# Kernel tuning notes

Measured on AMD Instinct MI355X. Metric: run time of the kernel, lower is better.

The kernel has to match this reference:

```python
import jax, jax.numpy as jnp
import numpy as np

B, S, D, H = 2, 2048, 1024, 16
DK = D // H

def setup_inputs() -> dict:
    key = jax.random.key(0)
    ks = jax.random.split(key, 8)
    scale = 1.0 / np.sqrt(D)
    return {
        "q": jax.random.normal(ks[0], (B, S, D), jnp.float32),
        "k": jax.random.normal(ks[1], (B, S, D), jnp.float32),
        "v": jax.random.normal(ks[2], (B, S, D), jnp.float32),
        "reaches": jax.random.uniform(ks[3], (B, S), jnp.float32),
        "Wq": jax.random.normal(ks[4], (D, D), jnp.float32) * scale,
        "Wk": jax.random.normal(ks[5], (D, D), jnp.float32) * scale,
        "Wv": jax.random.normal(ks[6], (D, D), jnp.float32) * scale,
        "Wo": jax.random.normal(ks[7], (D, D), jnp.float32) * scale,
    }

def _split_heads(x):
    # [B,S,D] -> [B,H,S,DK]
    return x.reshape(B, S, H, DK).transpose(0, 2, 1, 3)

def reference(q, k, v, reaches, Wq, Wk, Wv, Wo):
    # torch Linear: y = x @ W.T
    qh = _split_heads(q @ Wq.T)
    kh = _split_heads(k @ Wk.T)
    vh = _split_heads(v @ Wv.T)
    scores = jnp.einsum("bhqd,bhkd->bhqk", qh, kh) / jnp.sqrt(jnp.float32(DK))
    scores = jax.nn.softmax(scores, axis=-1)
    # post-softmax reach weighting along key axis
    scores = scores * reaches[:, None, None, :]
    # diagonal suppression: scores - scores*0.999999*eye
    scores = scores * (1.0 - 0.999999 * jnp.eye(S, dtype=scores.dtype))
    # inverted combine
    out = vh - jnp.einsum("bhqk,bhkd->bhqd", scores, vh)
    # per-position contribution rescale
    rs = reaches.sum(axis=-1, keepdims=True)
    contrib = (rs - reaches) / (rs + 1e-9) * (1.0 - reaches) * 100.0  # [B,S]
    out = out * contrib[:, None, :, None]
    concat = out.transpose(0, 2, 1, 3).reshape(B, S, D)
    return concat @ Wo.T
```

## Files before the change

### kernel.cpp

```cpp
#include <hip/hip_runtime.h>
#include <hip/hip_bf16.h>

typedef __attribute__((ext_vector_type(8))) short short8;
typedef __attribute__((ext_vector_type(4))) float f32x4;
typedef __attribute__((ext_vector_type(16))) float f32x16;
typedef unsigned short us;

#define B_ 2
#define S_ 2048
#define D_ 1024
#define H_ 16
#define DK_ 64
#define QSCALE 0.1803368867f

__device__ __forceinline__ us f2bf(float f) {
  union { float f; unsigned u; } x; x.f = f;
  unsigned r = x.u + 0x7FFFu + ((x.u >> 16) & 1u);
  return (us)(r >> 16);
}
__device__ __forceinline__ float bf2f(us h) {
  union { unsigned u; float f; } x; x.u = ((unsigned)h) << 16;
  return x.f;
}
__device__ __forceinline__ us f2bf_hw(float f) {
  __hip_bfloat16 h = __float2bfloat16(f);
  return *reinterpret_cast<us*>(&h);
}
__device__ __forceinline__ unsigned cvtpk(float lo, float hi) {
  unsigned r;
  asm("v_cvt_pk_bf16_f32 %0, %1, %2" : "=v"(r) : "v"(lo), "v"(hi));
  return r;
}

__device__ __forceinline__ void gload16(const void* g, void* l) {
  __builtin_amdgcn_global_load_lds((const __attribute__((address_space(1))) void*)g,
                                   (__attribute__((address_space(3))) void*)l, 16, 0, 0);
}

__global__ __launch_bounds__(256) void cvt_all(const float* __restrict__ q,
                                               const float* __restrict__ k,
                                               const float* __restrict__ v,
                                               const float* __restrict__ Wq,
                                               const float* __restrict__ Wk,
                                               const float* __restrict__ Wv,
                                               const float* __restrict__ Wo,
                                               const float* __restrict__ reaches,
                                               us* __restrict__ oq, us* __restrict__ ok,
                                               us* __restrict__ ov, us* __restrict__ oWq,
                                               us* __restrict__ oWk, us* __restrict__ oWv,
                                               us* __restrict__ oWo, float* __restrict__ rs) {
  int bid = blockIdx.x;
  if (bid >= 16384) {
    __shared__ float tmp[4];
    int t = threadIdx.x;
    for (int b = 0; b < B_; ++b) {
      float s = 0.f;
      for (int i = t; i < S_; i += 256) s += reaches[b * S_ + i];
      for (int o = 32; o > 0; o >>= 1) s += __shfl_down(s, o, 64);
      if ((t & 63) == 0) tmp[t >> 6] = s;
      __syncthreads();
      if (t == 0) rs[b] = tmp[0] + tmp[1] + tmp[2] + tmp[3];
      __syncthreads();
    }
    return;
  }
  const float* in; us* out; int off;
  if (bid < 12288) {
    int t = bid >> 12;
    in = (t == 0) ? q : (t == 1) ? k : v;
    out = (t == 0) ? oq : (t == 1) ? ok : ov;
    off = (bid & 4095) * 1024;
  } else {
    int t = (bid - 12288) >> 10;
    in = (t == 0) ? Wq : (t == 1) ? Wk : (t == 2) ? Wv : Wo;
    out = (t == 0) ? oWq : (t == 1) ? oWk : (t == 2) ? oWv : oWo;
    off = ((bid - 12288) & 1023) * 1024;
  }
  int i = off + threadIdx.x * 4;
  float4 val = *reinterpret_cast<const float4*>(in + i);
  ushort4 o;
  o.x = f2bf(val.x); o.y = f2bf(val.y); o.z = f2bf(val.z); o.w = f2bf(val.w);
  *reinterpret_cast<ushort4*>(out + i) = o;
}

__device__ __forceinline__ void gemm_core_hs(const us* __restrict__ A, const us* __restrict__ Bt,
                                             us* __restrict__ outH, float oscale) {
  __shared__ __align__(16) us lA[3][128 * 32];
  __shared__ __align__(16) us lB[3][128 * 32];
  const int tid = threadIdx.x;
  const int swz = (blockIdx.x & 7) * 32 + (blockIdx.x >> 3);
  const int bm = swz >> 3, bn = swz & 7;
  const int w = tid >> 6, lane = tid & 63;
  const int wr = (w >> 1) * 64, wc = (w & 1) * 64;
  const int lr = lane & 15, lg = lane >> 4;

  f32x4 acc[4][4];
#pragma unroll
  for (int i = 0; i < 4; ++i)
#pragma unroll
    for (int j = 0; j < 4; ++j) acc[i][j] = (f32x4){0.f, 0.f, 0.f, 0.f};

  const int crow = lane >> 2, ce8 = (lane & 3) * 8;
  const us* A0 = A + (size_t)(bm * 128 + w * 32 + crow) * 1024 + ce8;
  const us* A1 = A0 + (size_t)16 * 1024;
  const us* B0 = Bt + (size_t)(bn * 128 + w * 32 + crow) * 1024 + ce8;
  const us* B1 = B0 + (size_t)16 * 1024;
  const int dA0 = (w * 32) * 32, dA1 = (w * 32 + 16) * 32;

  gload16(A0, &lA[0][dA0]);
  gload16(A1, &lA[0][dA1]);
  gload16(B0, &lB[0][dA0]);
  gload16(B1, &lB[0][dA1]);

  int cur = 0, nxt = 1;
  for (int kt = 0; kt < 32; ++kt) {
    if (kt < 31) {
      int ko = (kt + 1) * 32;
      gload16(A0 + ko, &lA[nxt][dA0]);
      gload16(A1 + ko, &lA[nxt][dA1]);
      gload16(B0 + ko, &lB[nxt][dA0]);
      gload16(B1 + ko, &lB[nxt][dA1]);
      asm volatile("s_waitcnt vmcnt(4)" ::: "memory");
    } else {
      asm volatile("s_waitcnt vmcnt(0)" ::: "memory");
    }
    __builtin_amdgcn_s_barrier();
    __builtin_amdgcn_sched_barrier(0);

    short8 af[4], bfr[4];
#pragma unroll
    for (int i = 0; i < 4; ++i)
      af[i] = *reinterpret_cast<const short8*>(&lA[cur][(wr + i * 16 + lr) * 32 + lg * 8]);
#pragma unroll
    for (int j = 0; j < 4; ++j)
      bfr[j] = *reinterpret_cast<const short8*>(&lB[cur][(wc + j * 16 + lr) * 32 + lg * 8]);
    __builtin_amdgcn_s_setprio(1);
#pragma unroll
    for (int i = 0; i < 4; ++i)
#pragma unroll
      for (int j = 0; j < 4; ++j)
        acc[i][j] = __builtin_amdgcn_mfma_f32_16x16x32_bf16(af[i], bfr[j], acc[i][j], 0, 0, 0);
    __builtin_amdgcn_s_setprio(0);

    cur = nxt;
    nxt = (nxt == 2) ? 0 : nxt + 1;
  }
#pragma unroll
  for (int i = 0; i < 4; ++i)
#pragma unroll
    for (int j = 0; j < 4; ++j)
#pragma unroll
      for (int ii = 0; ii < 4; ++ii) {
        int r = bm * 128 + wr + i * 16 + lg * 4 + ii;
        int c = bn * 128 + wc + j * 16 + lr;
        float v = acc[i][j][ii] * oscale;
        int b = r >> 11, s = r & (S_ - 1), h = c >> 6, dk = c & 63;
        outH[(((size_t)(b * H_ + h) * S_ + s) * DK_) + dk] = f2bf(v);
      }
}

__global__ __launch_bounds__(256) void proj_gemm(const us* __restrict__ q_bf,
                                                 const us* __restrict__ k_bf,
                                                 const us* __restrict__ v_bf,
                                                 const us* __restrict__ Wq_bf,
                                                 const us* __restrict__ Wk_bf,
                                                 const us* __restrict__ Wv_bf,
                                                 us* __restrict__ Qh, us* __restrict__ Kh,
                                                 us* __restrict__ Vh) {
  if (blockIdx.y == 0) gemm_core_hs(q_bf, Wq_bf, Qh, QSCALE);
  else if (blockIdx.y == 1) gemm_core_hs(k_bf, Wk_bf, Kh, 1.0f);
  else gemm_core_hs(v_bf, Wv_bf, Vh, 1.0f);
}

__global__ __launch_bounds__(256) void wo_gemm(const us* __restrict__ A,
                                               const us* __restrict__ Bt,
                                               float* __restrict__ outF) {
  __shared__ __align__(16) us lA[3][128 * 32];
  __shared__ __align__(16) us lB[3][64 * 32];
  const int tid = threadIdx.x;
  const int swz = (blockIdx.x & 7) * 64 + (blockIdx.x >> 3);
  const int bm = swz >> 4, bn = swz & 15;
  const int w = tid >> 6, lane = tid & 63;
  const int lr = lane & 15, lg = lane >> 4;

  f32x4 acc[2][4];
#pragma unroll
  for (int i = 0; i < 2; ++i)
#pragma unroll
    for (int j = 0; j < 4; ++j) acc[i][j] = (f32x4){0.f, 0.f, 0.f, 0.f};

  const int crow = lane >> 2, ce8 = (lane & 3) * 8;
  const us* A0 = A + (size_t)(bm * 128 + w * 32 + crow) * 1024 + ce8;
  const us* A1 = A0 + (size_t)16 * 1024;
  const us* B0 = Bt + (size_t)(bn * 64 + w * 16 + crow) * 1024 + ce8;
  const int dA0 = (w * 32) * 32, dA1 = (w * 32 + 16) * 32, dB0 = (w * 16) * 32;

  gload16(A0, &lA[0][dA0]);
  gload16(A1, &lA[0][dA1]);
  gload16(B0, &lB[0][dB0]);

  int cur = 0, nxt = 1;
  for (int kt = 0; kt < 32; ++kt) {
    if (kt < 31) {
      int ko = (kt + 1) * 32;
      gload16(A0 + ko, &lA[nxt][dA0]);
      gload16(A1 + ko, &lA[nxt][dA1]);
      gload16(B0 + ko, &lB[nxt][dB0]);
      asm volatile("s_waitcnt vmcnt(3)" ::: "memory");
    } else {
      asm volatile("s_waitcnt vmcnt(0)" ::: "memory");
    }
    __builtin_amdgcn_s_barrier();
    __builtin_amdgcn_sched_barrier(0);

    short8 af[2], bfr[4];
#pragma unroll
    for (int i = 0; i < 2; ++i)
      af[i] = *reinterpret_cast<const short8*>(&lA[cur][(w * 32 + i * 16 + lr) * 32 + lg * 8]);
#pragma unroll
    for (int j = 0; j < 4; ++j)
      bfr[j] = *reinterpret_cast<const short8*>(&lB[cur][(j * 16 + lr) * 32 + lg * 8]);
    __builtin_amdgcn_s_setprio(1);
#pragma unroll
    for (int i = 0; i < 2; ++i)
#pragma unroll
      for (int j = 0; j < 4; ++j)
        acc[i][j] = __builtin_amdgcn_mfma_f32_16x16x32_bf16(af[i], bfr[j], acc[i][j], 0, 0, 0);
    __builtin_amdgcn_s_setprio(0);

    cur = nxt;
    nxt = (nxt == 2) ? 0 : nxt + 1;
  }
#pragma unroll
  for (int i = 0; i < 2; ++i)
#pragma unroll
    for (int j = 0; j < 4; ++j)
#pragma unroll
      for (int ii = 0; ii < 4; ++ii) {
        int r = bm * 128 + w * 32 + i * 16 + lg * 4 + ii;
        int c = bn * 64 + j * 16 + lr;
        outF[(size_t)r * 1024 + c] = acc[i][j][ii];
      }
}

__global__ __launch_bounds__(256) void transp_kernel(const us* __restrict__ Vh,
                                                     const float* __restrict__ reaches,
                                                     us* __restrict__ VhTw) {
  __shared__ us t[64 * 68];
  const int bh = blockIdx.x >> 5, st = blockIdx.x & 31;
  const int b = bh >> 4;
  const size_t base = (size_t)bh * S_ * DK_;
  const int r = threadIdx.x >> 3, e8 = (threadIdx.x & 7) * 8;
#pragma unroll
  for (int h2 = 0; h2 < 2; ++h2) {
    int row = r + h2 * 32;
    *reinterpret_cast<short8*>(&t[row * 68 + e8]) =
        *reinterpret_cast<const short8*>(&Vh[base + (size_t)(st * 64 + row) * DK_ + e8]);
  }
  __syncthreads();
#pragma unroll
  for (int h2 = 0; h2 < 2; ++h2) {
    int dk = (threadIdx.x >> 3) + h2 * 32;
    int sc = (threadIdx.x & 7) * 8;
    short8 v;
#pragma unroll
    for (int j = 0; j < 8; ++j) {
      float rw = reaches[b * S_ + st * 64 + sc + j];
      v[j] = (short)f2bf_hw(bf2f(t[(sc + j) * 68 + dk]) * rw);
    }
    *reinterpret_cast<short8*>(&VhTw[base + (size_t)dk * S_ + st * 64 + sc]) = v;
  }
}

__global__ __launch_bounds__(256, 2) void attn_kernel(const us* __restrict__ Qh,
                                                      const us* __restrict__ Kh,
                                                      const us* __restrict__ Vh,
                                                      const us* __restrict__ VhTw,
                                                      const float* __restrict__ reaches,
                                                      const float* __restrict__ rsum,
                                                      us* __restrict__ concat) {
  __shared__ __align__(16) us lK2[2][64 * 64];
  __shared__ __align__(16) us vT2[2][64 * 64];
  __shared__ float diagP[128];
  __shared__ float lsum[128];

  const int tid = threadIdx.x;
  const int bid = ((blockIdx.x & 7) << 6) | (blockIdx.x >> 3);
  const int qt = bid & 15;
  const int bh = bid >> 4;
  const int b = bh >> 4, h = bh & 15;
  const size_t base = (size_t)bh * S_ * DK_;

  const int w = tid >> 6, lane = tid & 63;
  const int l31 = lane & 31, hh = lane >> 5, l7 = lane & 7;
  const int h4 = hh * 4;
  const int r2 = tid >> 3, e8 = (tid & 7) * 8;
  const int diagkt = qt * 2 + (w >> 1);

  short8 aq[4];
  {
    const us* qp = &Qh[base + (size_t)(qt * 128 + w * 32 + l31) * DK_ + hh * 8];
#pragma unroll
    for (int dk = 0; dk < 4; ++dk)
      aq[dk] = *reinterpret_cast<const short8*>(qp + dk * 16);
  }

  int rdK[2][4];
#pragma unroll
  for (int c = 0; c < 2; ++c)
#pragma unroll
    for (int dk = 0; dk < 4; ++dk)
      rdK[c][dk] = (c * 32 + l31) * 64 + (((dk * 2 + hh) ^ l7) << 3);
  const int wslot = ((tid & 7) ^ (r2 & 7)) << 3;
  const int wK0 = r2 * 64 + wslot, wK1 = (r2 + 32) * 64 + wslot;

  short8 pk0, pk1, pv0, pv1;
  pk0 = *reinterpret_cast<const short8*>(&Kh[base + (size_t)r2 * DK_ + e8]);
  pk1 = *reinterpret_cast<const short8*>(&Kh[base + (size_t)(r2 + 32) * DK_ + e8]);
  pv0 = *reinterpret_cast<const short8*>(&VhTw[base + (size_t)r2 * S_ + e8]);
  pv1 = *reinterpret_cast<const short8*>(&VhTw[base + (size_t)(r2 + 32) * S_ + e8]);
  *reinterpret_cast<short8*>(&lK2[0][wK0]) = pk0;
  *reinterpret_cast<short8*>(&lK2[0][wK1]) = pk1;
  *reinterpret_cast<short8*>(&vT2[0][wK0]) = pv0;
  *reinterpret_cast<short8*>(&vT2[0][wK1]) = pv1;
  __syncthreads();

  f32x16 oacc[2];
  float lacc = 0.f;
#pragma unroll
  for (int c = 0; c < 2; ++c)
#pragma unroll
    for (int r = 0; r < 16; ++r) oacc[c][r] = 0.f;

  for (int kt = 0; kt < 32; ++kt) {
    const int cur = kt & 1;
    if (kt < 31) {
      int nt = kt + 1;
      pk0 = *reinterpret_cast<const short8*>(&Kh[base + (size_t)(nt * 64 + r2) * DK_ + e8]);
      pk1 = *reinterpret_cast<const short8*>(&Kh[base + (size_t)(nt * 64 + r2 + 32) * DK_ + e8]);
      pv0 = *reinterpret_cast<const short8*>(&VhTw[base + (size_t)r2 * S_ + nt * 64 + e8]);
      pv1 = *reinterpret_cast<const short8*>(&VhTw[base + (size_t)(r2 + 32) * S_ + nt * 64 + e8]);
    }

    f32x16 st0, st1;
#pragma unroll
    for (int r = 0; r < 16; ++r) { st0[r] = 0.f; st1[r] = 0.f; }
    __builtin_amdgcn_s_setprio(1);
#pragma unroll
    for (int dk = 0; dk < 4; ++dk) {
      short8 k0 = *reinterpret_cast<const short8*>(&lK2[cur][rdK[0][dk]]);
      st0 = __builtin_amdgcn_mfma_f32_32x32x16_bf16(k0, aq[dk], st0, 0, 0, 0);
      short8 k1 = *reinterpret_cast<const short8*>(&lK2[cur][rdK[1][dk]]);
      st1 = __builtin_amdgcn_mfma_f32_32x32x16_bf16(k1, aq[dk], st1, 0, 0, 0);
    }
    __builtin_amdgcn_s_setprio(0);

    float e0[16], e1[16];
#pragma unroll
    for (int r = 0; r < 16; ++r) {
      e0[r] = __builtin_amdgcn_exp2f(st0[r]);
      e1[r] = __builtin_amdgcn_exp2f(st1[r]);
      lacc += e0[r] + e1[r];
    }
    if (kt == diagkt) {
#pragma unroll
      for (int r = 0; r < 16; ++r) {
        int kk = (r & 3) + 8 * (r >> 2) + 4 * hh;
        float ev = (w & 1) ? e1[r] : e0[r];
        if (kk == l31) diagP[w * 32 + l31] = ev;
      }
    }

    short8 pa[4];
#pragma unroll
    for (int ks = 0; ks < 4; ++ks) {
      const int ro = (ks & 1) * 8;
      unsigned d0, s0, d1, s1;
      if (ks < 2) {
        d0 = cvtpk(e0[ro + 0], e0[ro + 1]);
        s0 = cvtpk(e0[ro + 4], e0[ro + 5]);
        d1 = cvtpk(e0[ro + 2], e0[ro + 3]);
        s1 = cvtpk(e0[ro + 6], e0[ro + 7]);
      } else {
        d0 = cvtpk(e1[ro + 0], e1[ro + 1]);
        s0 = cvtpk(e1[ro + 4], e1[ro + 5]);
        d1 = cvtpk(e1[ro + 2], e1[ro + 3]);
        s1 = cvtpk(e1[ro + 6], e1[ro + 7]);
      }
      asm("v_permlane32_swap_b32 %0, %1" : "+v"(d0), "+v"(s0));
      asm("v_permlane32_swap_b32 %0, %1" : "+v"(d1), "+v"(s1));
      union { unsigned u[4]; short8 v; } pk;
      pk.u[0] = d0; pk.u[1] = d1; pk.u[2] = s0; pk.u[3] = s1;
      pa[ks] = pk.v;
    }

    __builtin_amdgcn_s_setprio(1);
#pragma unroll
    for (int dc = 0; dc < 2; ++dc)
#pragma unroll
      for (int ks = 0; ks < 4; ++ks) {
        short8 bv = *reinterpret_cast<const short8*>(&vT2[cur][rdK[dc][ks]]);
        oacc[dc] = __builtin_amdgcn_mfma_f32_32x32x16_bf16(pa[ks], bv, oacc[dc], 0, 0, 0);
      }
    __builtin_amdgcn_s_setprio(0);

    if (kt < 31) {
      const int nx = cur ^ 1;
      *reinterpret_cast<short8*>(&lK2[nx][wK0]) = pk0;
      *reinterpret_cast<short8*>(&lK2[nx][wK1]) = pk1;
      *reinterpret_cast<short8*>(&vT2[nx][wK0]) = pv0;
      *reinterpret_cast<short8*>(&vT2[nx][wK1]) = pv1;
    }
    __syncthreads();
  }

  lacc += __shfl_xor(lacc, 32, 64);
  if (hh == 0) lsum[w * 32 + l31] = lacc;
  __syncthreads();

  const float rb = rsum[b];
#pragma unroll
  for (int r = 0; r < 16; ++r) {
    const int q = w * 32 + (r & 3) + 8 * (r >> 2) + h4;
    const int qg = qt * 128 + q;
    const float rq = reaches[b * S_ + qg];
    const float contrib = (rb - rq) / (rb + 1e-9f) * (1.f - rq) * 100.f;
    const float corr = 0.999999f * diagP[q] * rq;
    const float linv = 1.0f / lsum[q];
#pragma unroll
    for (int dc = 0; dc < 2; ++dc) {
      int d = dc * 32 + l31;
      float vhv = bf2f(Vh[base + (size_t)qg * DK_ + d]);
      float pv = (oacc[dc][r] - corr * vhv) * linv;
      float o = (vhv - pv) * contrib;
      concat[((size_t)(b * S_ + qg)) * D_ + h * 64 + d] = f2bf(o);
    }
  }
}

extern "C" void kernel_launch(void* const* d_in, const int* in_sizes, int n_in,
                              void* d_out, int out_size, void* d_ws, size_t ws_size,
                              hipStream_t stream) {
  const float* q = (const float*)d_in[0];
  const float* k = (const float*)d_in[1];
  const float* v = (const float*)d_in[2];
  const float* reaches = (const float*)d_in[3];
  const float* Wq = (const float*)d_in[4];
  const float* Wk = (const float*)d_in[5];
  const float* Wv = (const float*)d_in[6];
  const float* Wo = (const float*)d_in[7];

  const size_t NQKV = (size_t)B_ * S_ * D_;
  const size_t NW = (size_t)D_ * D_;

  us* q_bf = (us*)d_ws;
  us* k_bf = q_bf + NQKV;
  us* v_bf = k_bf + NQKV;
  us* Wq_bf = v_bf + NQKV;
  us* Wk_bf = Wq_bf + NW;
  us* Wv_bf = Wk_bf + NW;
  us* Wo_bf = Wv_bf + NW;
  us* Qh = Wo_bf + NW;
  us* Kh = Qh + NQKV;
  us* Vh = Kh + NQKV;
  us* concat = Vh + NQKV;
  float* rs = (float*)(concat + NQKV);
  us* VhTw = q_bf;

  cvt_all<<<16385, 256, 0, stream>>>(q, k, v, Wq, Wk, Wv, Wo, reaches,
                                     q_bf, k_bf, v_bf, Wq_bf, Wk_bf, Wv_bf, Wo_bf, rs);

  proj_gemm<<<dim3(256, 3), 256, 0, stream>>>(q_bf, k_bf, v_bf, Wq_bf, Wk_bf, Wv_bf, Qh, Kh, Vh);
  transp_kernel<<<B_ * H_ * (S_ / 64), 256, 0, stream>>>(Vh, reaches, VhTw);

  attn_kernel<<<B_ * H_ * (S_ / 128), 256, 0, stream>>>(Qh, Kh, Vh, VhTw, reaches, rs, concat);

  wo_gemm<<<512, 256, 0, stream>>>(concat, Wo_bf, (float*)d_out);
}
```

Measured before the change: 127.2 us.

## Fuse reach-weighted V transpose into V projection GEMM epilogue

```diff
diff --git a/kernel.cpp b/kernel.cpp
--- a/kernel.cpp
+++ b/kernel.cpp
@@ -84,9 +84,10 @@
 }
 
 __device__ __forceinline__ void gemm_core_hs(const us* __restrict__ A, const us* __restrict__ Bt,
-                                             us* __restrict__ outH, float oscale) {
-  __shared__ __align__(16) us lA[3][128 * 32];
-  __shared__ __align__(16) us lB[3][128 * 32];
+                                             us* __restrict__ outH, float oscale,
+                                             const float* __restrict__ reaches,
+                                             us* __restrict__ VhTw, int dov) {
+  __shared__ __align__(16) us smem[3][8192];
   const int tid = threadIdx.x;
   const int swz = (blockIdx.x & 7) * 32 + (blockIdx.x >> 3);
   const int bm = swz >> 3, bn = swz & 7;
@@ -107,19 +108,19 @@
   const us* B1 = B0 + (size_t)16 * 1024;
   const int dA0 = (w * 32) * 32, dA1 = (w * 32 + 16) * 32;
 
-  gload16(A0, &lA[0][dA0]);
-  gload16(A1, &lA[0][dA1]);
-  gload16(B0, &lB[0][dA0]);
-  gload16(B1, &lB[0][dA1]);
+  gload16(A0, &smem[0][dA0]);
+  gload16(A1, &smem[0][dA1]);
+  gload16(B0, &smem[0][4096 + dA0]);
+  gload16(B1, &smem[0][4096 + dA1]);
 
   int cur = 0, nxt = 1;
   for (int kt = 0; kt < 32; ++kt) {
     if (kt < 31) {
       int ko = (kt + 1) * 32;
-      gload16(A0 + ko, &lA[nxt][dA0]);
-      gload16(A1 + ko, &lA[nxt][dA1]);
-      gload16(B0 + ko, &lB[nxt][dA0]);
-      gload16(B1 + ko, &lB[nxt][dA1]);
+      gload16(A0 + ko, &smem[nxt][dA0]);
+      gload16(A1 + ko, &smem[nxt][dA1]);
+      gload16(B0 + ko, &smem[nxt][4096 + dA0]);
+      gload16(B1 + ko, &smem[nxt][4096 + dA1]);
       asm volatile("s_waitcnt vmcnt(4)" ::: "memory");
     } else {
       asm volatile("s_waitcnt vmcnt(0)" ::: "memory");
@@ -130,10 +131,10 @@
     short8 af[4], bfr[4];
 #pragma unroll
     for (int i = 0; i < 4; ++i)
-      af[i] = *reinterpret_cast<const short8*>(&lA[cur][(wr + i * 16 + lr) * 32 + lg * 8]);
+      af[i] = *reinterpret_cast<const short8*>(&smem[cur][(wr + i * 16 + lr) * 32 + lg * 8]);
 #pragma unroll
     for (int j = 0; j < 4; ++j)
-      bfr[j] = *reinterpret_cast<const short8*>(&lB[cur][(wc + j * 16 + lr) * 32 + lg * 8]);
+      bfr[j] = *reinterpret_cast<const short8*>(&smem[cur][4096 + (wc + j * 16 + lr) * 32 + lg * 8]);
     __builtin_amdgcn_s_setprio(1);
 #pragma unroll
     for (int i = 0; i < 4; ++i)
@@ -145,18 +146,53 @@
     cur = nxt;
     nxt = (nxt == 2) ? 0 : nxt + 1;
   }
+
+  us* tbuf = &smem[0][0];
+  if (dov) __syncthreads();
+
 #pragma unroll
   for (int i = 0; i < 4; ++i)
 #pragma unroll
     for (int j = 0; j < 4; ++j)
 #pragma unroll
       for (int ii = 0; ii < 4; ++ii) {
-        int r = bm * 128 + wr + i * 16 + lg * 4 + ii;
-        int c = bn * 128 + wc + j * 16 + lr;
+        int rl = wr + i * 16 + lg * 4 + ii;
+        int cl = wc + j * 16 + lr;
+        int r = bm * 128 + rl;
+        int c = bn * 128 + cl;
         float v = acc[i][j][ii] * oscale;
         int b = r >> 11, s = r & (S_ - 1), h = c >> 6, dk = c & 63;
-        outH[(((size_t)(b * H_ + h) * S_ + s) * DK_) + dk] = f2bf(v);
+        us bv = f2bf(v);
+        outH[(((size_t)(b * H_ + h) * S_ + s) * DK_) + dk] = bv;
+        if (dov) tbuf[cl * 136 + rl] = bv;
       }
+
+  if (dov) {
+    __syncthreads();
+    const int dl = tid >> 1, s0q = (tid & 1) * 64;
+    const int bq = bm >> 4;
+    const int bh = bq * 16 + bn * 2 + (dl >> 6);
+    const int dk = dl & 63;
+    const int sbase = (bm & 15) * 128 + s0q;
+    const size_t ob = (size_t)bh * DK_ * S_ + (size_t)dk * S_ + sbase;
+    const float* rp = reaches + bq * S_ + sbase;
+#pragma unroll
+    for (int k8 = 0; k8 < 8; ++k8) {
+      short8 vv = *reinterpret_cast<const short8*>(&tbuf[dl * 136 + s0q + k8 * 8]);
+      float4 ra = *reinterpret_cast<const float4*>(rp + k8 * 8);
+      float4 rb = *reinterpret_cast<const float4*>(rp + k8 * 8 + 4);
+      short8 ov;
+      ov[0] = (short)f2bf_hw(bf2f((us)vv[0]) * ra.x);
+      ov[1] = (short)f2bf_hw(bf2f((us)vv[1]) * ra.y);
+      ov[2] = (short)f2bf_hw(bf2f((us)vv[2]) * ra.z);
+      ov[3] = (short)f2bf_hw(bf2f((us)vv[3]) * ra.w);
+      ov[4] = (short)f2bf_hw(bf2f((us)vv[4]) * rb.x);
+      ov[5] = (short)f2bf_hw(bf2f((us)vv[5]) * rb.y);
+      ov[6] = (short)f2bf_hw(bf2f((us)vv[6]) * rb.z);
+      ov[7] = (short)f2bf_hw(bf2f((us)vv[7]) * rb.w);
+      *reinterpret_cast<short8*>(&VhTw[ob + k8 * 8]) = ov;
+    }
+  }
 }
 
 __global__ __launch_bounds__(256) void proj_gemm(const us* __restrict__ q_bf,
@@ -166,10 +202,12 @@
                                                  const us* __restrict__ Wk_bf,
                                                  const us* __restrict__ Wv_bf,
                                                  us* __restrict__ Qh, us* __restrict__ Kh,
-                                                 us* __restrict__ Vh) {
-  if (blockIdx.y == 0) gemm_core_hs(q_bf, Wq_bf, Qh, QSCALE);
-  else if (blockIdx.y == 1) gemm_core_hs(k_bf, Wk_bf, Kh, 1.0f);
-  else gemm_core_hs(v_bf, Wv_bf, Vh, 1.0f);
+                                                 us* __restrict__ Vh,
+                                                 const float* __restrict__ reaches,
+                                                 us* __restrict__ VhTw, int dov) {
+  if (blockIdx.y == 0) gemm_core_hs(q_bf, Wq_bf, Qh, QSCALE, nullptr, nullptr, 0);
+  else if (blockIdx.y == 1) gemm_core_hs(k_bf, Wk_bf, Kh, 1.0f, nullptr, nullptr, 0);
+  else gemm_core_hs(v_bf, Wv_bf, Vh, 1.0f, reaches, VhTw, dov);
 }
 
 __global__ __launch_bounds__(256) void wo_gemm(const us* __restrict__ A,
@@ -465,13 +503,19 @@
   us* Vh = Kh + NQKV;
   us* concat = Vh + NQKV;
   float* rs = (float*)(concat + NQKV);
-  us* VhTw = q_bf;
+
+  us* vt_new = (us*)(rs + 4);
+  size_t need = (size_t)((char*)(vt_new + NQKV) - (char*)d_ws);
+  int fused = (ws_size >= need) ? 1 : 0;
+  us* VhTw = fused ? vt_new : q_bf;
 
   cvt_all<<<16385, 256, 0, stream>>>(q, k, v, Wq, Wk, Wv, Wo, reaches,
                                      q_bf, k_bf, v_bf, Wq_bf, Wk_bf, Wv_bf, Wo_bf, rs);
 
-  proj_gemm<<<dim3(256, 3), 256, 0, stream>>>(q_bf, k_bf, v_bf, Wq_bf, Wk_bf, Wv_bf, Qh, Kh, Vh);
-  transp_kernel<<<B_ * H_ * (S_ / 64), 256, 0, stream>>>(Vh, reaches, VhTw);
+  proj_gemm<<<dim3(256, 3), 256, 0, stream>>>(q_bf, k_bf, v_bf, Wq_bf, Wk_bf, Wv_bf,
+                                              Qh, Kh, Vh, reaches, VhTw, fused);
+  if (!fused)
+    transp_kernel<<<B_ * H_ * (S_ / 64), 256, 0, stream>>>(Vh, reaches, VhTw);
 
   attn_kernel<<<B_ * H_ * (S_ / 128), 256, 0, stream>>>(Qh, Kh, Vh, VhTw, reaches, rs, concat);
 
```

Result: slower. 134.2 us (+5.5%).
